# Performance work log

Hardware: AMD Instinct MI355X
Metric: run time of the kernel (lower is better)

The kernel has to match this reference:

```python
import jax, jax.numpy as jnp
import numpy as np

DT = 0.5
T_STEPS = int(2500 / DT)   # 5000
T_STIM = int(2000 / DT)    # 4000
A = 270.0; B_ = 108.0; D_ = 0.154; GAMMA = 0.641; TAU_S = 100.0; TAU_AMPA = 2.0
BATCH = 4096


def setup_inputs() -> dict:
    key = jax.random.key(0)
    k0, k1, k2, k3, k4 = jax.random.split(key, 5)
    return {
        "input_signal": jax.random.normal(k0, (BATCH, 1), dtype=jnp.float32),
        "J11": jnp.float32(0.2609), "J12": jnp.float32(0.0497),
        "J21": jnp.float32(0.0497), "J22": jnp.float32(0.2609),
        "J_ext": jnp.float32(0.0156), "I_0": jnp.float32(0.3255),
        "noise_ampa": jnp.float32(0.02), "threshold": jnp.float32(0.5),
        "motor_delay": jnp.float32(0.1),
        "eps0_1": jax.random.normal(k1, (BATCH, 1), dtype=jnp.float32),
        "eps0_2": jax.random.normal(k2, (BATCH, 1), dtype=jnp.float32),
        "eps_1": jax.random.normal(k3, (T_STEPS, BATCH, 1), dtype=jnp.float32),
        "eps_2": jax.random.normal(k4, (T_STEPS, BATCH, 1), dtype=jnp.float32),
    }


def _H(x):
    # Wong-Wang f-I curve: relu((a x - b) / (1 - exp(-d (a x - b)) + 1e-6))
    u = A * x - B_
    return jax.nn.relu(u / (1.0 - jnp.exp(-D_ * u) + 1e-6))


def _simulate(input_signal, J11, J12, J21, J22, J_ext, I_0, noise_ampa,
              eps0_1, eps0_2, eps_1, eps_2):
    decay = jnp.exp(jnp.float32(-DT / TAU_AMPA))
    nscale = jnp.float32(np.sqrt((1.0 - np.exp(-2.0 * DT / TAU_AMPA)) / 2.0))
    s0 = jnp.full_like(input_signal, 0.1)  # [B,1]
    carry0 = (s0, s0, eps0_1 * noise_ampa, eps0_2 * noise_ampa)

    def step(carry, xs):
        s1, s2, In1, In2 = carry
        e1, e2, t = xs
        stim = t < T_STIM
        I1 = jnp.where(stim, J_ext * (1.0 + input_signal / 100.0), 0.0)
        I2 = jnp.where(stim, J_ext * (1.0 - input_signal / 100.0), 0.0)
        x1 = J11 * s1 - J12 * s2 + I_0 + I1 + In1
        x2 = J22 * s2 - J21 * s1 + I_0 + I2 + In2
        ds1 = -(s1 / TAU_S) + (1.0 - s1) * _H(x1) * GAMMA / 1000.0
        ds2 = -(s2 / TAU_S) + (1.0 - s2) * _H(x2) * GAMMA / 1000.0
        In1n = In1 * decay + noise_ampa * nscale * e1
        In2n = In2 * decay + noise_ampa * nscale * e2
        s1n = s1 + ds1 * DT
        s2n = s2 + ds2 * DT
        ys = (jnp.concatenate([s1n, s2n], axis=-1),   # trajectory row [B,2]
              jnp.concatenate([ds1, ds2], axis=-1))   # dsdt row [B,2]
        return (s1n, s2n, In1n, In2n), ys

    ts = jnp.arange(T_STEPS)
    _, (traj, dsdt) = jax.lax.scan(step, carry0, (eps_1, eps_2, ts))
    return traj, dsdt  # each [T, B, 2]


def _decide(traj_m):
    # traj_m = trajectory - threshold; first-crossing times per unit
    m1 = traj_m[:, :, 0] > 0
    m2 = traj_m[:, :, 1] > 0
    inf = jnp.float32(jnp.inf)
    t1 = jnp.where(m1.any(0), jnp.argmax(m1, axis=0).astype(jnp.float32), inf)
    t2 = jnp.where(m2.any(0), jnp.argmax(m2, axis=0).astype(jnp.float32), inf)
    dtimes = jnp.where(t1 < t2, t1, -t2)
    return dtimes * DT


def reference(input_signal, J11, J12, J21, J22, J_ext, I_0, noise_ampa,
              threshold, motor_delay, eps0_1, eps0_2, eps_1, eps_2):
    traj, dsdt = _simulate(input_signal, J11, J12, J21, J22, J_ext, I_0,
                           noise_ampa, eps0_1, eps0_2, eps_1, eps_2)
    out = _decide(traj - threshold)  # [B], signed decision time in ms
    out = jnp.where(out < 0, out / 1000.0 - motor_delay,
                    jnp.where(out > 0, out / 1000.0 + motor_delay, out))
    return out
```

## Files before the change

### kernel.cpp

```cpp
#include <hip/hip_runtime.h>

#define BATCHN 4096
#define NSTEPS 5000
#define NSTIM  4000
#define U      25
#define NBLK      (NSTEPS / U)
#define NBLK_STIM (NSTIM / U)

__global__ __launch_bounds__(128, 1) void ww_kernel(
    const float* __restrict__ input_signal,
    const float* __restrict__ sJ11, const float* __restrict__ sJ12,
    const float* __restrict__ sJ21, const float* __restrict__ sJ22,
    const float* __restrict__ sJext, const float* __restrict__ sI0,
    const float* __restrict__ sNoise, const float* __restrict__ sThr,
    const float* __restrict__ sDelay,
    const float* __restrict__ eps0_1, const float* __restrict__ eps0_2,
    const float* __restrict__ eps_1, const float* __restrict__ eps_2,
    float* __restrict__ out)
{
    __shared__ float4 slab[2][U][64];
    __shared__ int flag;

    const int tid  = threadIdx.x;
    const int lane = tid & 63;
    const int b    = blockIdx.x * 64 + lane;

    const float noise = sNoise[0];
    const float Jext = sJext[0], I0 = sI0[0];
    const float KE = -0.22217503629690245f;

    const float inp = input_signal[b];
    const float P1s = fmaf(270.0f, I0 + Jext * (1.0f + inp * 0.01f), -108.0f);
    const float P2s = fmaf(270.0f, I0 + Jext * (1.0f - inp * 0.01f), -108.0f);
    const float Pn  = fmaf(270.0f, I0, -108.0f);

    if (tid >= 64) {
        const float decay = 0.7788007830714049f;
        const float kN270 = noise * 0.4435478165294536f * 270.0f;
        const float* __restrict__ p1 = eps_1 + b;
        const float* __restrict__ p2 = eps_2 + b;
        float V1 = eps0_1[b] * noise * 270.0f;
        float V2 = eps0_2[b] * noise * 270.0f;

        auto fill = [&](int blk) {
            const int sl = blk & 1;
            const size_t off = (size_t)blk * U * BATCHN;
            const bool stim = (blk < NBLK_STIM);
            const float P1 = stim ? P1s : Pn;
            const float P2 = stim ? P2s : Pn;
            float r1[U], r2[U];
            #pragma unroll
            for (int i = 0; i < U; ++i) {
                r1[i] = p1[off + (size_t)i * BATCHN];
                r2[i] = p2[off + (size_t)i * BATCHN];
            }
            #pragma unroll
            for (int i = 0; i < U; ++i) {
                float C1 = V1 + P1;
                float C2 = V2 + P2;
                slab[sl][i][lane] = make_float4(C1, C2, KE * C1, KE * C2);
                V1 = fmaf(V1, decay, kN270 * r1[i]);
                V2 = fmaf(V2, decay, kN270 * r2[i]);
            }
        };

        fill(0);
        __syncthreads();
        for (int blk = 0; blk < NBLK; ++blk) {
            if (blk + 1 < NBLK) fill(blk + 1);
            __syncthreads();
            if (flag) break;
        }
        return;
    }

    __builtin_amdgcn_s_setprio(3);
    const float J11 = sJ11[0], J12 = sJ12[0], J21 = sJ21[0], J22 = sJ22[0];
    const float thr = sThr[0], delay = sDelay[0];

    const float A11 = 270.0f * J11, nA12 = -270.0f * J12;
    const float A22 = 270.0f * J22, nA21 = -270.0f * J21;
    const float B11 = KE * A11, B12 = KE * nA12;
    const float B22 = KE * A22, B21 = KE * nA21;
    const float SM = 0.995f;
    const float QC = 3.205e-4f;
    const float INF = __builtin_inff();

    float s1 = 0.1f, s2 = 0.1f;
    float tm1 = INF, tm2 = INF;
    float tf = 0.0f;

    if (tid == 0) flag = 0;
    __syncthreads();
    bool done = false;
    for (int blk = 0; blk < NBLK && !done; ++blk) {
        const float4* __restrict__ base = &slab[blk & 1][0][lane];
        float4 d0 = base[0];
        float4 d1 = base[64];
        #pragma unroll
        for (int i = 0; i < U; ++i) {
            float4 cu = d0;
            d0 = d1;
            if (i + 2 < U) d1 = base[(i + 2) * 64];
            float u1 = fmaf(A11, s1, fmaf(nA12, s2, cu.x));
            float u2 = fmaf(A22, s2, fmaf(nA21, s1, cu.y));
            float w1 = fmaf(B11, s1, fmaf(B12, s2, cu.z));
            float w2 = fmaf(B22, s2, fmaf(B21, s1, cu.w));
            float x1 = __builtin_amdgcn_exp2f(w1);
            float x2 = __builtin_amdgcn_exp2f(w2);
            float r1 = __builtin_amdgcn_rcpf(1.000001f - x1);
            float r2 = __builtin_amdgcn_rcpf(1.000001f - x2);
            float h1 = fmaxf(u1 * r1, 0.0f);
            float h2 = fmaxf(u2 * r2, 0.0f);
            s1 = fmaf(h1, fmaf(-QC, s1, QC), SM * s1);
            s2 = fmaf(h2, fmaf(-QC, s2, QC), SM * s2);
            tm1 = fminf(tm1, (s1 > thr) ? tf : INF);
            tm2 = fminf(tm2, (s2 > thr) ? tf : INF);
            tf += 1.0f;
        }
        done = __all((tm1 < INF) || (tm2 < INF));
        if (done && lane == 0) flag = 1;
        __syncthreads();
    }

    float o;
    if (tm1 == INF && tm2 == INF) {
        o = -3.0e38f;
    } else {
        float dtm = (tm1 < tm2) ? tm1 : -tm2;
        o = dtm * 0.5f;
        if (o < 0.0f)      o = o / 1000.0f - delay;
        else if (o > 0.0f) o = o / 1000.0f + delay;
    }
    out[b] = o;
}

extern "C" void kernel_launch(void* const* d_in, const int* in_sizes, int n_in,
                              void* d_out, int out_size, void* d_ws, size_t ws_size,
                              hipStream_t stream) {
    ww_kernel<<<dim3(BATCHN / 64), dim3(128), 0, stream>>>(
        (const float*)d_in[0],
        (const float*)d_in[1],
        (const float*)d_in[2],
        (const float*)d_in[3],
        (const float*)d_in[4],
        (const float*)d_in[5],
        (const float*)d_in[6],
        (const float*)d_in[7],
        (const float*)d_in[8],
        (const float*)d_in[9],
        (const float*)d_in[10],
        (const float*)d_in[11],
        (const float*)d_in[12],
        (const float*)d_in[13],
        (float*)d_out);
}
```

Baseline: 471.7 us.

## Interleave two batch sets per compute wave and offload threshold scan to producers

Each block now has one compute wave that advances two independent 64-element batch sets at once, fed by two producer waves. Interleaving two recurrence chains is meant to hide the exp2/rcp latency of the serial time loop. The producers now stage pre-scaled inputs as float2 and also scan the stored trajectories for threshold crossings. A shared exit-block handshake coordinates early termination. The separate u term is dropped by folding the KE scale into the reciprocal, and the grid shrinks to half as many blocks, which trades more work per wave for fewer active CUs.

```diff
diff --git a/kernel.cpp b/kernel.cpp
--- a/kernel.cpp
+++ b/kernel.cpp
@@ -6,8 +6,9 @@
 #define U      25
 #define NBLK      (NSTEPS / U)
 #define NBLK_STIM (NSTIM / U)
-
-__global__ __launch_bounds__(128, 1) void ww_kernel(
+#define BPB    128
+
+__global__ __launch_bounds__(192, 1) void ww_kernel(
     const float* __restrict__ input_signal,
     const float* __restrict__ sJ11, const float* __restrict__ sJ12,
     const float* __restrict__ sJ21, const float* __restrict__ sJ22,
@@ -18,110 +19,153 @@
     const float* __restrict__ eps_1, const float* __restrict__ eps_2,
     float* __restrict__ out)
 {
-    __shared__ float4 slab[2][U][64];
-    __shared__ int flag;
+    __shared__ float2 slab[2][2][U][64];
+    __shared__ float2 strc[2][2][U][64];
+    __shared__ int done2[2];
+    __shared__ int exit_blk;
 
     const int tid  = threadIdx.x;
     const int lane = tid & 63;
-    const int b    = blockIdx.x * 64 + lane;
-
+    const int wave = tid >> 6;
+
+    const float KE = -0.22217503629690245f;
+
+    if (wave == 0) {
+        __builtin_amdgcn_s_setprio(3);
+        const float J11 = sJ11[0], J12 = sJ12[0], J21 = sJ21[0], J22 = sJ22[0];
+        const float B11 = KE * 270.0f * J11, B12 = -KE * 270.0f * J12;
+        const float B22 = KE * 270.0f * J22, B21 = -KE * 270.0f * J21;
+        const float nKE  = -KE;
+        const float KE1p = 1.000001f * KE;
+        const float SM = 0.995f;
+        const float QC = 3.205e-4f;
+
+        float s1a = 0.1f, s2a = 0.1f;
+        float s1b = 0.1f, s2b = 0.1f;
+
+        if (lane == 0) { done2[0] = 0; done2[1] = 0; exit_blk = 0x7fffffff; }
+        __syncthreads();
+        bool wrote = false;
+        for (int blk = 0; blk < NBLK; ++blk) {
+            if (blk >= *(volatile int*)&exit_blk) break;
+            if (!wrote && *(volatile int*)&done2[0] && *(volatile int*)&done2[1]) {
+                if (lane == 0) exit_blk = blk + 1;
+                wrote = true;
+            }
+            const int sl = blk & 1;
+            const float2* __restrict__ bA = &slab[0][sl][0][lane];
+            const float2* __restrict__ bB = &slab[1][sl][0][lane];
+            float2* __restrict__ tA = &strc[0][sl][0][lane];
+            float2* __restrict__ tB = &strc[1][sl][0][lane];
+            float2 a0 = bA[0], a1 = bA[64];
+            float2 b0 = bB[0], b1 = bB[64];
+            #pragma unroll
+            for (int i = 0; i < U; ++i) {
+                float2 ka = a0; a0 = a1;
+                float2 kb = b0; b0 = b1;
+                if (i + 2 < U) { a1 = bA[(i + 2) * 64]; b1 = bB[(i + 2) * 64]; }
+                float w1a = fmaf(B11, s1a, fmaf(B12, s2a, ka.x));
+                float w2a = fmaf(B22, s2a, fmaf(B21, s1a, ka.y));
+                float w1b = fmaf(B11, s1b, fmaf(B12, s2b, kb.x));
+                float w2b = fmaf(B22, s2b, fmaf(B21, s1b, kb.y));
+                float x1a = __builtin_amdgcn_exp2f(w1a);
+                float x2a = __builtin_amdgcn_exp2f(w2a);
+                float x1b = __builtin_amdgcn_exp2f(w1b);
+                float x2b = __builtin_amdgcn_exp2f(w2b);
+                float r1a = __builtin_amdgcn_rcpf(fmaf(nKE, x1a, KE1p));
+                float r2a = __builtin_amdgcn_rcpf(fmaf(nKE, x2a, KE1p));
+                float r1b = __builtin_amdgcn_rcpf(fmaf(nKE, x1b, KE1p));
+                float r2b = __builtin_amdgcn_rcpf(fmaf(nKE, x2b, KE1p));
+                float h1a = fmaxf(w1a * r1a, 0.0f);
+                float h2a = fmaxf(w2a * r2a, 0.0f);
+                float h1b = fmaxf(w1b * r1b, 0.0f);
+                float h2b = fmaxf(w2b * r2b, 0.0f);
+                s1a = fmaf(h1a, fmaf(-QC, s1a, QC), SM * s1a);
+                s2a = fmaf(h2a, fmaf(-QC, s2a, QC), SM * s2a);
+                s1b = fmaf(h1b, fmaf(-QC, s1b, QC), SM * s1b);
+                s2b = fmaf(h2b, fmaf(-QC, s2b, QC), SM * s2b);
+                tA[i * 64] = make_float2(s1a, s2a);
+                tB[i * 64] = make_float2(s1b, s2b);
+            }
+            __syncthreads();
+        }
+        return;
+    }
+
+    const int set = wave - 1;
+    const int b   = blockIdx.x * BPB + set * 64 + lane;
     const float noise = sNoise[0];
     const float Jext = sJext[0], I0 = sI0[0];
-    const float KE = -0.22217503629690245f;
+    const float thr = sThr[0], delay = sDelay[0];
 
     const float inp = input_signal[b];
     const float P1s = fmaf(270.0f, I0 + Jext * (1.0f + inp * 0.01f), -108.0f);
     const float P2s = fmaf(270.0f, I0 + Jext * (1.0f - inp * 0.01f), -108.0f);
     const float Pn  = fmaf(270.0f, I0, -108.0f);
-
-    if (tid >= 64) {
-        const float decay = 0.7788007830714049f;
-        const float kN270 = noise * 0.4435478165294536f * 270.0f;
-        const float* __restrict__ p1 = eps_1 + b;
-        const float* __restrict__ p2 = eps_2 + b;
-        float V1 = eps0_1[b] * noise * 270.0f;
-        float V2 = eps0_2[b] * noise * 270.0f;
-
-        auto fill = [&](int blk) {
-            const int sl = blk & 1;
-            const size_t off = (size_t)blk * U * BATCHN;
-            const bool stim = (blk < NBLK_STIM);
-            const float P1 = stim ? P1s : Pn;
-            const float P2 = stim ? P2s : Pn;
-            float r1[U], r2[U];
-            #pragma unroll
-            for (int i = 0; i < U; ++i) {
-                r1[i] = p1[off + (size_t)i * BATCHN];
-                r2[i] = p2[off + (size_t)i * BATCHN];
-            }
-            #pragma unroll
-            for (int i = 0; i < U; ++i) {
-                float C1 = V1 + P1;
-                float C2 = V2 + P2;
-                slab[sl][i][lane] = make_float4(C1, C2, KE * C1, KE * C2);
-                V1 = fmaf(V1, decay, kN270 * r1[i]);
-                V2 = fmaf(V2, decay, kN270 * r2[i]);
-            }
-        };
-
-        fill(0);
-        __syncthreads();
-        for (int blk = 0; blk < NBLK; ++blk) {
-            if (blk + 1 < NBLK) fill(blk + 1);
-            __syncthreads();
-            if (flag) break;
-        }
-        return;
-    }
-
-    __builtin_amdgcn_s_setprio(3);
-    const float J11 = sJ11[0], J12 = sJ12[0], J21 = sJ21[0], J22 = sJ22[0];
-    const float thr = sThr[0], delay = sDelay[0];
-
-    const float A11 = 270.0f * J11, nA12 = -270.0f * J12;
-    const float A22 = 270.0f * J22, nA21 = -270.0f * J21;
-    const float B11 = KE * A11, B12 = KE * nA12;
-    const float B22 = KE * A22, B21 = KE * nA21;
-    const float SM = 0.995f;
-    const float QC = 3.205e-4f;
+    const float KP1s = KE * P1s, KP2s = KE * P2s, KPn = KE * Pn;
+
+    const float decay = 0.7788007830714049f;
+    const float kKE   = KE * noise * 0.4435478165294536f * 270.0f;
+    const float n270K = noise * 270.0f * KE;
+
+    const float* __restrict__ p1 = eps_1 + b;
+    const float* __restrict__ p2 = eps_2 + b;
+    float VK1 = eps0_1[b] * n270K;
+    float VK2 = eps0_2[b] * n270K;
+
+    auto fill = [&](int blk) {
+        const int sl = blk & 1;
+        const size_t off = (size_t)blk * U * BATCHN;
+        const bool stim = (blk < NBLK_STIM);
+        const float KP1 = stim ? KP1s : KPn;
+        const float KP2 = stim ? KP2s : KPn;
+        float2* __restrict__ dst = &slab[set][sl][0][lane];
+        float r1[U], r2[U];
+        #pragma unroll
+        for (int i = 0; i < U; ++i) {
+            r1[i] = p1[off + (size_t)i * BATCHN];
+            r2[i] = p2[off + (size_t)i * BATCHN];
+        }
+        #pragma unroll
+        for (int i = 0; i < U; ++i) {
+            dst[i * 64] = make_float2(VK1 + KP1, VK2 + KP2);
+            VK1 = fmaf(VK1, decay, kKE * r1[i]);
+            VK2 = fmaf(VK2, decay, kKE * r2[i]);
+        }
+    };
+
     const float INF = __builtin_inff();
-
-    float s1 = 0.1f, s2 = 0.1f;
     float tm1 = INF, tm2 = INF;
     float tf = 0.0f;
-
-    if (tid == 0) flag = 0;
-    __syncthreads();
-    bool done = false;
-    for (int blk = 0; blk < NBLK && !done; ++blk) {
-        const float4* __restrict__ base = &slab[blk & 1][0][lane];
-        float4 d0 = base[0];
-        float4 d1 = base[64];
+    bool mydone = false;
+
+    auto scan = [&](int blk) {
+        const int sl = blk & 1;
+        const float2* __restrict__ src = &strc[set][sl][0][lane];
         #pragma unroll
         for (int i = 0; i < U; ++i) {
-            float4 cu = d0;
-            d0 = d1;
-            if (i + 2 < U) d1 = base[(i + 2) * 64];
-            float u1 = fmaf(A11, s1, fmaf(nA12, s2, cu.x));
-            float u2 = fmaf(A22, s2, fmaf(nA21, s1, cu.y));
-            float w1 = fmaf(B11, s1, fmaf(B12, s2, cu.z));
-            float w2 = fmaf(B22, s2, fmaf(B21, s1, cu.w));
-            float x1 = __builtin_amdgcn_exp2f(w1);
-            float x2 = __builtin_amdgcn_exp2f(w2);
-            float r1 = __builtin_amdgcn_rcpf(1.000001f - x1);
-            float r2 = __builtin_amdgcn_rcpf(1.000001f - x2);
-            float h1 = fmaxf(u1 * r1, 0.0f);
-            float h2 = fmaxf(u2 * r2, 0.0f);
-            s1 = fmaf(h1, fmaf(-QC, s1, QC), SM * s1);
-            s2 = fmaf(h2, fmaf(-QC, s2, QC), SM * s2);
-            tm1 = fminf(tm1, (s1 > thr) ? tf : INF);
-            tm2 = fminf(tm2, (s2 > thr) ? tf : INF);
+            float2 sv = src[i * 64];
+            tm1 = fminf(tm1, (sv.x > thr) ? tf : INF);
+            tm2 = fminf(tm2, (sv.y > thr) ? tf : INF);
             tf += 1.0f;
         }
-        done = __all((tm1 < INF) || (tm2 < INF));
-        if (done && lane == 0) flag = 1;
+    };
+
+    fill(0);
+    __syncthreads();
+    for (int blk = 0; blk < NBLK; ++blk) {
+        if (blk >= *(volatile int*)&exit_blk) break;
+        if (blk + 1 < NBLK) fill(blk + 1);
+        if (blk >= 1) {
+            scan(blk - 1);
+            if (!mydone && __all((tm1 < INF) || (tm2 < INF))) {
+                if (lane == 0) done2[set] = 1;
+                mydone = true;
+            }
+        }
         __syncthreads();
     }
+    if (!mydone) scan(NBLK - 1);
 
     float o;
     if (tm1 == INF && tm2 == INF) {
@@ -138,7 +182,7 @@
 extern "C" void kernel_launch(void* const* d_in, const int* in_sizes, int n_in,
                               void* d_out, int out_size, void* d_ws, size_t ws_size,
                               hipStream_t stream) {
-    ww_kernel<<<dim3(BATCHN / 64), dim3(128), 0, stream>>>(
+    ww_kernel<<<dim3(BATCHN / BPB), dim3(192), 0, stream>>>(
         (const float*)d_in[0],
         (const float*)d_in[1],
         (const float*)d_in[2],
```

Result: slower. 651.1 us (+38.0%).
